# Optimization experiments

Measured on AMD Instinct MI355X. Metric: run time of the kernel, lower is better.

The kernel has to match this reference:

```python
import jax, jax.numpy as jnp
import numpy as np
from jax import lax

ALPHA = 100.0          # SuperSpike surrogate slope (method='super', alpha=100)
DT_TAU_MEM = 0.1       # dt * tau_mem_inv = 0.001 * 100
DT_TAU_SYN = 0.2       # dt * tau_syn_inv = 0.001 * 200
V_TH = 1.0
SEQ = 40

@jax.custom_vjp
def spike(x):
    return (x > 0).astype(x.dtype)

def _spike_fwd(x):
    return (x > 0).astype(x.dtype), x

def _spike_bwd(x, g):
    # SuperSpike surrogate gradient: 1 / (alpha*|x| + 1)^2
    return (g / (ALPHA * jnp.abs(x) + 1.0) ** 2,)

spike.defvjp(_spike_fwd, _spike_bwd)

def encode(current):
    # ConstantCurrentLIFEncoder: LIF driven by constant current, SEQ steps.
    def step(v, _):
        v = v + DT_TAU_MEM * (-v + current)   # v_leak = 0
        z = spike(v - V_TH)
        v = v * (1.0 - z)                     # v_reset = 0
        return v, z
    _, zs = lax.scan(step, jnp.zeros_like(current), None, length=SEQ)
    return zs  # (SEQ, B, F)

def setup_inputs() -> dict:
    key = jax.random.key(0)
    ks = jax.random.split(key, 5)
    B = 16384
    x = jax.random.normal(ks[0], (B, 4), jnp.float32)
    w_in = jax.random.normal(ks[1], (128, 8), jnp.float32) * np.sqrt(2.0 / 8)
    w_rec = jax.random.normal(ks[2], (128, 128), jnp.float32) * np.sqrt(2.0 / 128)
    w_out = jax.random.normal(ks[3], (2, 128), jnp.float32) * np.sqrt(2.0 / 128)
    keep = jax.random.bernoulli(ks[4], 0.5, (SEQ, B, 128))
    dropout_mask = keep.astype(jnp.float32) * 2.0  # inverted dropout, p=0.5
    return {"x": x, "w_in": w_in, "w_rec": w_rec, "w_out": w_out,
            "dropout_mask": dropout_mask}

def reference(x, w_in, w_rec, w_out, dropout_mask):
    scale = 50.0
    x_pos = encode(jax.nn.relu(scale * x))     # (T, B, 4)
    x_neg = encode(jax.nn.relu(-scale * x))    # (T, B, 4)
    xs = jnp.concatenate([x_pos, x_neg], axis=2)  # (T, B, 8)

    B = x.shape[0]
    H = w_rec.shape[0]
    O = w_out.shape[0]
    z0 = jnp.zeros((B, H), x.dtype)
    v0 = jnp.zeros((B, H), x.dtype)
    i0 = jnp.zeros((B, H), x.dtype)
    vo0 = jnp.zeros((B, O), x.dtype)
    io0 = jnp.zeros((B, O), x.dtype)

    def step(carry, inp):
        z, v, i, vo, io = carry
        xt, mt = inp
        # LIFCell (recurrent)
        v_dec = v + DT_TAU_MEM * (-v + i)
        i_dec = i * (1.0 - DT_TAU_SYN)
        z_new = spike(v_dec - V_TH)
        v_new = (1.0 - z_new) * v_dec
        i_new = i_dec + xt @ w_in.T + z @ w_rec.T
        # Dropout on spikes
        z_d = z_new * mt
        # LICell readout
        vo_new = vo + DT_TAU_MEM * (-vo + io)
        io_new = io * (1.0 - DT_TAU_SYN) + z_d @ w_out.T
        return (z_new, v_new, i_new, vo_new, io_new), vo_new

    _, voltages = lax.scan(step, (z0, v0, i0, vo0, io0), (xs, dropout_mask))
    m = jnp.max(voltages, axis=0)          # (B, O)
    return jax.nn.softmax(m, axis=1)
```

## Files before the change

### kernel.cpp

```cpp
#include <hip/hip_runtime.h>
#include <cstdint>

#define T_SEQ 40
#define NB    16384
#define NH    128
#define ZSTR  168
#define GROWS 16
#define NTHR  256
#define NBLK  (NB / GROWS)

typedef float v4f __attribute__((ext_vector_type(4)));
typedef short v8s __attribute__((ext_vector_type(8)));

__device__ __forceinline__ unsigned short f2bf(float f) {
  uint32_t u = __float_as_uint(f);
  return (unsigned short)((u + 0x7FFFu + ((u >> 16) & 1u)) >> 16);
}
__device__ __forceinline__ float bf2f(unsigned short b) {
  return __uint_as_float(((uint32_t)b) << 16);
}
template <int C>
__device__ __forceinline__ float dppadd(float v) {
  int t = __builtin_amdgcn_update_dpp(0, __float_as_int(v), C, 0xF, 0xF, true);
  return v + __int_as_float(t);
}
__device__ __forceinline__ float red16(float v) {
  v = dppadd<0x111>(v);
  v = dppadd<0x112>(v);
  v = dppadd<0x114>(v);
  v = dppadd<0x118>(v);
  return v;
}

__global__ __launch_bounds__(NTHR, 2)
void Policy_22033182228693_kernel(const float* __restrict__ x,
                                  const float* __restrict__ w_in,
                                  const float* __restrict__ w_rec,
                                  const float* __restrict__ w_out,
                                  const float* __restrict__ dmask,
                                  float* __restrict__ out)
{
  __shared__ unsigned short Z[2][GROWS * ZSTR];
  __shared__ unsigned short XS[T_SEQ * 128];
  __shared__ float UP[2][4][GROWS][2];
  __shared__ float MF[GROWS][2];

  const int tid  = threadIdx.x;
  const int wv   = tid >> 6;
  const int lane = tid & 63;
  const int m    = lane & 15;
  const int q    = lane >> 4;
  const int wcol = wv * 32;
  const int gb   = blockIdx.x * GROWS;

  v8s bfr[2][5][3];
#pragma unroll
  for (int tau = 0; tau < 2; ++tau) {
    const int n = wcol + tau * 16 + m;
#pragma unroll
    for (int c = 0; c < 5; ++c) {
      const int kb = c * 32 + q * 8;
      union { v8s v; unsigned short u[8]; } f0, f1, f2;
#pragma unroll
      for (int j = 0; j < 8; ++j) {
        const int k = kb + j;
        float w = (k < NH)  ? w_rec[n * NH + k]
                : (k < 136) ? w_in[n * 8 + (k - NH)] : 0.f;
        unsigned short b1 = f2bf(w);  float r1 = w - bf2f(b1);
        unsigned short b2 = f2bf(r1); float r2 = r1 - bf2f(b2);
        unsigned short b3 = f2bf(r2);
        f0.u[j] = b1; f1.u[j] = b2; f2.u[j] = b3;
      }
      bfr[tau][c][0] = f0.v; bfr[tau][c][1] = f1.v; bfr[tau][c][2] = f2.v;
    }
  }

  const float wo00 = w_out[wcol + m],      wo01 = w_out[wcol + 16 + m];
  const float wo10 = w_out[NH + wcol + m], wo11 = w_out[NH + wcol + 16 + m];

  for (int e = tid; e < 2 * GROWS * ZSTR; e += NTHR) ((unsigned short*)Z)[e] = 0;
  __syncthreads();

  if (tid < 128) {
    const int bi = tid >> 3, ch = tid & 7;
    float xv = x[(size_t)(gb + bi) * 4 + (ch & 3)];
    float cc = fmaxf(0.f, ((ch & 4) ? -50.f : 50.f) * xv);
    float ve = 0.f;
    for (int t = 0; t < T_SEQ; ++t) {
      ve += 0.1f * (cc - ve);
      unsigned short zb = 0;
      if (ve > 1.0f) { zb = 0x3F80; ve = 0.f; }
      XS[t * 128 + tid] = zb;
      if (t == 0) Z[0][bi * ZSTR + NH + ch] = zb;
    }
  }
  __syncthreads();

  v4f iacc[2] = {{0,0,0,0},{0,0,0,0}};
  v4f vmem[2] = {{0,0,0,0},{0,0,0,0}};
  float io = 0.f, vo = 0.f, mx = -3.0e38f;
  const size_t TS = (size_t)NB * NH;
  int pb = 0;

#pragma unroll 1
  for (int t = 0; t < T_SEQ; ++t) {
    float mk[2][4];
#pragma unroll
    for (int tau = 0; tau < 2; ++tau)
#pragma unroll
      for (int r = 0; r < 4; ++r)
        mk[tau][r] = dmask[(size_t)t * TS + (size_t)(gb + q * 4 + r) * NH + wcol + tau * 16 + m];

    v8s af[5];
    const unsigned short* zrow = &Z[pb][m * ZSTR];
#pragma unroll
    for (int c = 0; c < 5; ++c) af[c] = *(const v8s*)(zrow + c * 32 + q * 8);

    float zf[2][4];
#pragma unroll
    for (int tau = 0; tau < 2; ++tau) {
      v4f vd = vmem[tau] + 0.1f * (iacc[tau] - vmem[tau]);
#pragma unroll
      for (int r = 0; r < 4; ++r) {
        bool z = vd[r] > 1.0f;
        zf[tau][r] = z ? 1.0f : 0.0f;
        vmem[tau][r] = z ? 0.0f : vd[r];
      }
    }

    v4f a0 = 0.8f * iacc[0];
    v4f a1 = 0.8f * iacc[1];
#pragma unroll
    for (int s = 0; s < 3; ++s)
#pragma unroll
      for (int c = 0; c < 5; ++c) {
        a0 = __builtin_amdgcn_mfma_f32_16x16x32_bf16(af[c], bfr[0][c][s], a0, 0, 0, 0);
        a1 = __builtin_amdgcn_mfma_f32_16x16x32_bf16(af[c], bfr[1][c][s], a1, 0, 0, 0);
      }
    iacc[0] = a0; iacc[1] = a1;

    unsigned short* zq = &Z[pb ^ 1][0];
#pragma unroll
    for (int tau = 0; tau < 2; ++tau)
#pragma unroll
      for (int r = 0; r < 4; ++r)
        zq[(q * 4 + r) * ZSTR + wcol + tau * 16 + m] = (zf[tau][r] != 0.f) ? 0x3F80 : 0;

    if (t + 1 < T_SEQ && tid >= 128) {
      const int u = tid - 128;
      Z[pb ^ 1][(u >> 3) * ZSTR + NH + (u & 7)] = XS[(t + 1) * 128 + u];
    }

#pragma unroll
    for (int r = 0; r < 4; ++r) {
      float zd0 = zf[0][r] * mk[0][r];
      float zd1 = zf[1][r] * mk[1][r];
      float p0 = zd0 * wo00 + zd1 * wo01;
      float p1 = zd0 * wo10 + zd1 * wo11;
      p0 = red16(p0);
      p1 = red16(p1);
      if (m == 15) {
        UP[t & 1][wv][q * 4 + r][0] = p0;
        UP[t & 1][wv][q * 4 + r][1] = p1;
      }
    }

    __syncthreads();

    if (wv == 0 && lane < 32) {
      const int row = lane >> 1, o = lane & 1;
      float u = UP[t & 1][0][row][o] + UP[t & 1][1][row][o]
              + UP[t & 1][2][row][o] + UP[t & 1][3][row][o];
      float von = vo + 0.1f * (io - vo);
      io = 0.8f * io + u;
      vo = von;
      mx = fmaxf(mx, vo);
    }
    pb ^= 1;
  }

  __syncthreads();
  if (wv == 0 && lane < 32) MF[lane >> 1][lane & 1] = mx;
  __syncthreads();
  if (tid < GROWS) {
    float a = MF[tid][0], b = MF[tid][1];
    float mxx = fmaxf(a, b);
    float e0 = expf(a - mxx), e1 = expf(b - mxx);
    float inv = 1.f / (e0 + e1);
    ((float2*)out)[gb + tid] = make_float2(e0 * inv, e1 * inv);
  }
}

extern "C" void kernel_launch(void* const* d_in, const int* in_sizes, int n_in,
                              void* d_out, int out_size, void* d_ws, size_t ws_size,
                              hipStream_t stream) {
  const float* x     = (const float*)d_in[0];
  const float* w_in  = (const float*)d_in[1];
  const float* w_rec = (const float*)d_in[2];
  const float* w_out = (const float*)d_in[3];
  const float* dmask = (const float*)d_in[4];
  float* out = (float*)d_out;

  hipLaunchKernelGGL(Policy_22033182228693_kernel, dim3(NBLK), dim3(NTHR), 0, stream,
                     x, w_in, w_rec, w_out, dmask, out);
}
```

Before: 460.7 us.

## Prefetch dropout mask into LDS, split MFMA chains, defer readout integration

Dropout-mask loads for step t+1 are now issued as coalesced float4 loads into a double-buffered LDS tile during step t, replacing strided per-lane global loads that sat on the critical path. The three bf16-split MFMA accumulation chains are given independent accumulators so they can interleave, at the cost of small extra adds. Per-step readout partials are stored for all timesteps and the LI readout recurrence runs once after the loop, which removes wave-0 serial work from every step. Weight loading is vectorized. LDS use grows with the full-sequence UP buffer and the mask tile, which could reduce occupancy.

```diff
diff --git a/kernel.cpp b/kernel.cpp
--- a/kernel.cpp
+++ b/kernel.cpp
@@ -42,8 +42,8 @@
 {
   __shared__ unsigned short Z[2][GROWS * ZSTR];
   __shared__ unsigned short XS[T_SEQ * 128];
-  __shared__ float UP[2][4][GROWS][2];
-  __shared__ float MF[GROWS][2];
+  __shared__ float MB[2][GROWS * NH];
+  __shared__ float UP[T_SEQ][4][GROWS][2];
 
   const int tid  = threadIdx.x;
   const int wv   = tid >> 6;
@@ -52,6 +52,7 @@
   const int q    = lane >> 4;
   const int wcol = wv * 32;
   const int gb   = blockIdx.x * GROWS;
+  const size_t TS = (size_t)NB * NH;
 
   v8s bfr[2][5][3];
 #pragma unroll
@@ -60,12 +61,25 @@
 #pragma unroll
     for (int c = 0; c < 5; ++c) {
       const int kb = c * 32 + q * 8;
+      float w8[8];
+      if (c < 4) {
+        float4 wa = *(const float4*)&w_rec[n * NH + kb];
+        float4 wb = *(const float4*)&w_rec[n * NH + kb + 4];
+        w8[0]=wa.x; w8[1]=wa.y; w8[2]=wa.z; w8[3]=wa.w;
+        w8[4]=wb.x; w8[5]=wb.y; w8[6]=wb.z; w8[7]=wb.w;
+      } else if (q == 0) {
+        float4 wa = *(const float4*)&w_in[n * 8];
+        float4 wb = *(const float4*)&w_in[n * 8 + 4];
+        w8[0]=wa.x; w8[1]=wa.y; w8[2]=wa.z; w8[3]=wa.w;
+        w8[4]=wb.x; w8[5]=wb.y; w8[6]=wb.z; w8[7]=wb.w;
+      } else {
+#pragma unroll
+        for (int j = 0; j < 8; ++j) w8[j] = 0.f;
+      }
       union { v8s v; unsigned short u[8]; } f0, f1, f2;
 #pragma unroll
       for (int j = 0; j < 8; ++j) {
-        const int k = kb + j;
-        float w = (k < NH)  ? w_rec[n * NH + k]
-                : (k < 136) ? w_in[n * 8 + (k - NH)] : 0.f;
+        float w = w8[j];
         unsigned short b1 = f2bf(w);  float r1 = w - bf2f(b1);
         unsigned short b2 = f2bf(r1); float r2 = r1 - bf2f(b2);
         unsigned short b3 = f2bf(r2);
@@ -81,35 +95,41 @@
   for (int e = tid; e < 2 * GROWS * ZSTR; e += NTHR) ((unsigned short*)Z)[e] = 0;
   __syncthreads();
 
-  if (tid < 128) {
-    const int bi = tid >> 3, ch = tid & 7;
-    float xv = x[(size_t)(gb + bi) * 4 + (ch & 3)];
-    float cc = fmaxf(0.f, ((ch & 4) ? -50.f : 50.f) * xv);
-    float ve = 0.f;
-    for (int t = 0; t < T_SEQ; ++t) {
-      ve += 0.1f * (cc - ve);
-      unsigned short zb = 0;
-      if (ve > 1.0f) { zb = 0x3F80; ve = 0.f; }
-      XS[t * 128 + tid] = zb;
-      if (t == 0) Z[0][bi * ZSTR + NH + ch] = zb;
-    }
+  const int srow = tid >> 4;
+  const int scol = (tid & 15) * 8;
+  {
+    const float* g0 = dmask + (size_t)(gb + srow) * NH + scol;
+    float4 p0 = *(const float4*)g0;
+    float4 p1 = *(const float4*)(g0 + 4);
+    if (tid < 128) {
+      const int bi = tid >> 3, ch = tid & 7;
+      float xv = x[(size_t)(gb + bi) * 4 + (ch & 3)];
+      float cc = fmaxf(0.f, ((ch & 4) ? -50.f : 50.f) * xv);
+      float ve = 0.f;
+      for (int t = 0; t < T_SEQ; ++t) {
+        ve += 0.1f * (cc - ve);
+        unsigned short zb = 0;
+        if (ve > 1.0f) { zb = 0x3F80; ve = 0.f; }
+        XS[t * 128 + tid] = zb;
+        if (t == 0) Z[0][bi * ZSTR + NH + ch] = zb;
+      }
+    }
+    float* mrow = &MB[0][srow * NH + scol];
+    *(float4*)mrow = p0;
+    *(float4*)(mrow + 4) = p1;
   }
   __syncthreads();
 
   v4f iacc[2] = {{0,0,0,0},{0,0,0,0}};
   v4f vmem[2] = {{0,0,0,0},{0,0,0,0}};
-  float io = 0.f, vo = 0.f, mx = -3.0e38f;
-  const size_t TS = (size_t)NB * NH;
   int pb = 0;
 
 #pragma unroll 1
   for (int t = 0; t < T_SEQ; ++t) {
-    float mk[2][4];
-#pragma unroll
-    for (int tau = 0; tau < 2; ++tau)
-#pragma unroll
-      for (int r = 0; r < 4; ++r)
-        mk[tau][r] = dmask[(size_t)t * TS + (size_t)(gb + q * 4 + r) * NH + wcol + tau * 16 + m];
+    const int tn = (t + 1 < T_SEQ) ? t + 1 : T_SEQ - 1;
+    const float* gs = dmask + (size_t)tn * TS + (size_t)(gb + srow) * NH + scol;
+    float4 npf0 = *(const float4*)gs;
+    float4 npf1 = *(const float4*)(gs + 4);
 
     v8s af[5];
     const unsigned short* zrow = &Z[pb][m * ZSTR];
@@ -128,16 +148,19 @@
       }
     }
 
-    v4f a0 = 0.8f * iacc[0];
-    v4f a1 = 0.8f * iacc[1];
-#pragma unroll
-    for (int s = 0; s < 3; ++s)
-#pragma unroll
-      for (int c = 0; c < 5; ++c) {
-        a0 = __builtin_amdgcn_mfma_f32_16x16x32_bf16(af[c], bfr[0][c][s], a0, 0, 0, 0);
-        a1 = __builtin_amdgcn_mfma_f32_16x16x32_bf16(af[c], bfr[1][c][s], a1, 0, 0, 0);
-      }
-    iacc[0] = a0; iacc[1] = a1;
+    v4f s00 = 0.8f * iacc[0], s01 = {0,0,0,0}, s02 = {0,0,0,0};
+    v4f s10 = 0.8f * iacc[1], s11 = {0,0,0,0}, s12 = {0,0,0,0};
+#pragma unroll
+    for (int c = 0; c < 5; ++c) {
+      s00 = __builtin_amdgcn_mfma_f32_16x16x32_bf16(af[c], bfr[0][c][0], s00, 0, 0, 0);
+      s10 = __builtin_amdgcn_mfma_f32_16x16x32_bf16(af[c], bfr[1][c][0], s10, 0, 0, 0);
+      s01 = __builtin_amdgcn_mfma_f32_16x16x32_bf16(af[c], bfr[0][c][1], s01, 0, 0, 0);
+      s11 = __builtin_amdgcn_mfma_f32_16x16x32_bf16(af[c], bfr[1][c][1], s11, 0, 0, 0);
+      s02 = __builtin_amdgcn_mfma_f32_16x16x32_bf16(af[c], bfr[0][c][2], s02, 0, 0, 0);
+      s12 = __builtin_amdgcn_mfma_f32_16x16x32_bf16(af[c], bfr[1][c][2], s12, 0, 0, 0);
+    }
+    iacc[0] = (s00 + s01) + s02;
+    iacc[1] = (s10 + s11) + s12;
 
     unsigned short* zq = &Z[pb ^ 1][0];
 #pragma unroll
@@ -153,41 +176,49 @@
 
 #pragma unroll
     for (int r = 0; r < 4; ++r) {
-      float zd0 = zf[0][r] * mk[0][r];
-      float zd1 = zf[1][r] * mk[1][r];
+      float mk0 = MB[t & 1][(q * 4 + r) * NH + wcol + m];
+      float mk1 = MB[t & 1][(q * 4 + r) * NH + wcol + 16 + m];
+      float zd0 = zf[0][r] * mk0;
+      float zd1 = zf[1][r] * mk1;
       float p0 = zd0 * wo00 + zd1 * wo01;
       float p1 = zd0 * wo10 + zd1 * wo11;
       p0 = red16(p0);
       p1 = red16(p1);
       if (m == 15) {
-        UP[t & 1][wv][q * 4 + r][0] = p0;
-        UP[t & 1][wv][q * 4 + r][1] = p1;
-      }
+        UP[t][wv][q * 4 + r][0] = p0;
+        UP[t][wv][q * 4 + r][1] = p1;
+      }
+    }
+
+    {
+      float* mrow = &MB[(t + 1) & 1][srow * NH + scol];
+      *(float4*)mrow = npf0;
+      *(float4*)(mrow + 4) = npf1;
     }
 
     __syncthreads();
-
-    if (wv == 0 && lane < 32) {
-      const int row = lane >> 1, o = lane & 1;
-      float u = UP[t & 1][0][row][o] + UP[t & 1][1][row][o]
-              + UP[t & 1][2][row][o] + UP[t & 1][3][row][o];
+    pb ^= 1;
+  }
+
+  if (tid < 32) {
+    const int row = tid >> 1, o = tid & 1;
+    float io = 0.f, vo = 0.f, mx = -3.0e38f;
+#pragma unroll 1
+    for (int t = 0; t < T_SEQ; ++t) {
+      float u = ((UP[t][0][row][o] + UP[t][1][row][o])
+               +  UP[t][2][row][o]) + UP[t][3][row][o];
       float von = vo + 0.1f * (io - vo);
       io = 0.8f * io + u;
       vo = von;
       mx = fmaxf(mx, vo);
     }
-    pb ^= 1;
-  }
-
-  __syncthreads();
-  if (wv == 0 && lane < 32) MF[lane >> 1][lane & 1] = mx;
-  __syncthreads();
-  if (tid < GROWS) {
-    float a = MF[tid][0], b = MF[tid][1];
-    float mxx = fmaxf(a, b);
-    float e0 = expf(a - mxx), e1 = expf(b - mxx);
-    float inv = 1.f / (e0 + e1);
-    ((float2*)out)[gb + tid] = make_float2(e0 * inv, e1 * inv);
+    float other = __shfl_xor(mx, 1);
+    if (o == 0) {
+      float mxx = fmaxf(mx, other);
+      float e0 = expf(mx - mxx), e1 = expf(other - mxx);
+      float inv = 1.f / (e0 + e1);
+      ((float2*)out)[gb + row] = make_float2(e0 * inv, e1 * inv);
+    }
   }
 }
 
```

New measurement: 472.4 us. +2.5%, slower.
